# Optimization experiments

Measured on AMD Instinct MI355X. Metric: run time of the kernel, lower is better.

The kernel has to match this reference:

```python
import jax, jax.numpy as jnp
import numpy as np

N = 100000   # nodes
E = 1600000  # edges
D = 128      # in_channels
H = 128      # hidden_dim
L = 3        # num_layers
LH = 128     # lstm_hidden
OUT = 16     # output_dim
G = 128      # graphs in batch
EPS = 1e-5   # BatchNorm eps


def setup_inputs() -> dict:
    key = jax.random.key(0)
    ks = jax.random.split(key, 14)
    x = jax.random.normal(ks[0], (N, D), jnp.float32)
    src = jax.random.randint(ks[1], (E,), 0, N)
    dst = jax.random.randint(ks[2], (E,), 0, N)
    edge_index = jnp.stack([src, dst])
    batch = jnp.sort(jax.random.randint(ks[3], (N,), 0, G))
    Ws = jax.random.normal(ks[4], (L, D, H), jnp.float32) / np.float32(np.sqrt(D))
    bs = jax.random.normal(ks[5], (L, H), jnp.float32) * 0.02
    gammas = 1.0 + 0.1 * jax.random.normal(ks[6], (L, H), jnp.float32)
    betas = 0.1 * jax.random.normal(ks[7], (L, H), jnp.float32)
    rms = 0.1 * jax.random.normal(ks[8], (L, H), jnp.float32)
    rvs = jax.random.uniform(ks[9], (L, H), jnp.float32, 0.5, 1.5)
    W_ih = jax.random.normal(ks[10], (4 * LH, H), jnp.float32) / np.float32(np.sqrt(H))
    W_hh = jax.random.normal(ks[11], (4 * LH, LH), jnp.float32) / np.float32(np.sqrt(LH))
    b_ih = jnp.zeros((4 * LH,), jnp.float32)
    b_hh = jnp.zeros((4 * LH,), jnp.float32)
    W_fc = jax.random.normal(ks[12], (OUT, LH), jnp.float32) / np.float32(np.sqrt(LH))
    b_fc = 0.02 * jax.random.normal(ks[13], (OUT,), jnp.float32)
    return dict(x=x, edge_index=edge_index, batch=batch, Ws=Ws, bs=bs,
                gammas=gammas, betas=betas, rms=rms, rvs=rvs,
                W_ih=W_ih, W_hh=W_hh, b_ih=b_ih, b_hh=b_hh, W_fc=W_fc, b_fc=b_fc)


def reference(x, edge_index, batch, Ws, bs, gammas, betas, rms, rvs,
              W_ih, W_hh, b_ih, b_hh, W_fc, b_fc):
    # GCNConv: add self-loops, symmetric deg^-1/2 normalization
    src, dst = edge_index[0], edge_index[1]
    loop = jnp.arange(N)
    s = jnp.concatenate([src, loop])
    d = jnp.concatenate([dst, loop])
    deg = jax.ops.segment_sum(jnp.ones((E + N,), x.dtype), d, num_segments=N)
    dinv = jax.lax.rsqrt(jnp.maximum(deg, 1.0))  # deg >= 1 due to self-loops
    norm = (dinv[s] * dinv[d])[:, None]          # [E+N, 1]
    h = x
    for l in range(L):
        h = h @ Ws[l]                                                  # [N, H]
        agg = jax.ops.segment_sum(h[s] * norm, d, num_segments=N) + bs[l]
        # BatchNorm (eval: running stats) -> dropout (eval: identity) -> ReLU
        y = (agg - rms[l]) * (gammas[l] * jax.lax.rsqrt(rvs[l] + EPS)) + betas[l]
        h = jax.nn.relu(y)
    # global_mean_pool
    sums = jax.ops.segment_sum(h, batch, num_segments=G)               # [G, H]
    cnt = jax.ops.segment_sum(jnp.ones((N,), h.dtype), batch, num_segments=G)
    pooled = sums / jnp.maximum(cnt, 1.0)[:, None]
    # single-timestep LSTM, h0 = c0 = 0 -> forget gate contributes nothing
    gates = pooled @ W_ih.T + b_ih + b_hh                              # [G, 4*LH]
    i, f, g, o = jnp.split(gates, 4, axis=-1)
    c = jax.nn.sigmoid(i) * jnp.tanh(g)
    hn = jax.nn.sigmoid(o) * jnp.tanh(c)
    return hn @ W_fc.T + b_fc                                          # [G, OUT]
```

## Files before the change

### kernel.cpp

```cpp
#include <hip/hip_runtime.h>
#include <math.h>

constexpr int   NN  = 100000;
constexpr int   EE  = 1600000;
constexpr int   HH  = 128;
constexpr int   GG  = 128;
constexpr float EPSV = 1e-5f;
constexpr int   NSB = 256;
constexpr int   SUBW = (NN + NSB - 1) / NSB;
constexpr int   CAP2 = 8192;
constexpr int   GEMM_BLOCKS = (NN + 127) / 128;

typedef __attribute__((ext_vector_type(8))) short  short8;
typedef __attribute__((ext_vector_type(4))) float  f32x4;
typedef __attribute__((ext_vector_type(2))) float  v2f;

__device__ __forceinline__ unsigned short f2bf(float f) {
    union { float f; unsigned u; } v; v.f = f;
    unsigned r = v.u + 0x7FFF + ((v.u >> 16) & 1);
    return (unsigned short)(r >> 16);
}
__device__ __forceinline__ float bf2f(unsigned short b) {
    union { unsigned u; float f; } v; v.u = ((unsigned)b) << 16;
    return v.f;
}

constexpr size_t A256(size_t x) { return (x + 255) & ~(size_t)255; }
constexpr size_t OFF_TL  = 0;
constexpr size_t OFF_DNV = A256(OFF_TL  + 256 * 4);
constexpr size_t OFF_RP  = A256(OFF_DNV + (size_t)NN * 4);
constexpr size_t OFF_SRC = A256(OFF_RP  + (size_t)(NN + 1) * 4);
constexpr size_t OFF_B2  = A256(OFF_SRC + (size_t)EE * 4);
constexpr size_t OFF_HW  = A256(OFF_B2  + (size_t)NSB * CAP2 * 4);
constexpr size_t OFF_H0  = A256(OFF_HW  + (size_t)NN * HH * 2);
constexpr size_t OFF_PL  = A256(OFF_H0  + (size_t)NN * HH * 2);

template<bool FP32A>
__device__ __forceinline__ void gemm_body(const void* __restrict__ Ap,
                                          const float* __restrict__ W,
                                          unsigned short* __restrict__ C,
                                          int nrows, int rb) {
    __shared__ unsigned short WtH[64 * 136];
    __shared__ unsigned short WtL[64 * 136];
    int t = threadIdx.x;
    int row0 = rb * 128;
    int wv = t >> 6, lane = t & 63, m = lane & 15, q = lane >> 4;
    long rowA = row0 + wv * 32 + m;
    long rowB = rowA + 16;

    short8 a[2][4];
#pragma unroll
    for (int kc = 0; kc < 4; ++kc) {
        int ko = kc * 32 + q * 8;
        if (FP32A) {
            const float* Af = (const float*)Ap;
            float4 f0 = {0,0,0,0}, f1 = {0,0,0,0}, g0 = {0,0,0,0}, g1 = {0,0,0,0};
            if (rowA < nrows) {
                f0 = *(const float4*)(Af + rowA * 128 + ko);
                f1 = *(const float4*)(Af + rowA * 128 + ko + 4);
            }
            if (rowB < nrows) {
                g0 = *(const float4*)(Af + rowB * 128 + ko);
                g1 = *(const float4*)(Af + rowB * 128 + ko + 4);
            }
            union { short8 s; unsigned short u[8]; } ua, ub;
            ua.u[0] = f2bf(f0.x); ua.u[1] = f2bf(f0.y); ua.u[2] = f2bf(f0.z); ua.u[3] = f2bf(f0.w);
            ua.u[4] = f2bf(f1.x); ua.u[5] = f2bf(f1.y); ua.u[6] = f2bf(f1.z); ua.u[7] = f2bf(f1.w);
            ub.u[0] = f2bf(g0.x); ub.u[1] = f2bf(g0.y); ub.u[2] = f2bf(g0.z); ub.u[3] = f2bf(g0.w);
            ub.u[4] = f2bf(g1.x); ub.u[5] = f2bf(g1.y); ub.u[6] = f2bf(g1.z); ub.u[7] = f2bf(g1.w);
            a[0][kc] = ua.s; a[1][kc] = ub.s;
        } else {
            const unsigned short* Ab = (const unsigned short*)Ap;
            short8 z = {};
            a[0][kc] = (rowA < nrows) ? *(const short8*)(Ab + rowA * 128 + ko) : z;
            a[1][kc] = (rowB < nrows) ? *(const short8*)(Ab + rowB * 128 + ko) : z;
        }
    }

    for (int half = 0; half < 2; ++half) {
        int c0 = half * 64;
        __syncthreads();
        for (int idx = t; idx < 64 * 128; idx += 256) {
            int k = idx >> 6, c = idx & 63;
            float w = W[k * 128 + c0 + c];
            unsigned short hb = f2bf(w);
            WtH[c * 136 + k] = hb;
            WtL[c * 136 + k] = f2bf(w - bf2f(hb));
        }
        __syncthreads();
        f32x4 acc[2][4] = {};
#pragma unroll
        for (int kc = 0; kc < 4; ++kc) {
            int ko = kc * 32 + q * 8;
#pragma unroll
            for (int ct = 0; ct < 4; ++ct) {
                short8 bh = *(const short8*)(WtH + (ct * 16 + m) * 136 + ko);
                short8 bl = *(const short8*)(WtL + (ct * 16 + m) * 136 + ko);
                acc[0][ct] = __builtin_amdgcn_mfma_f32_16x16x32_bf16(a[0][kc], bh, acc[0][ct], 0, 0, 0);
                acc[0][ct] = __builtin_amdgcn_mfma_f32_16x16x32_bf16(a[0][kc], bl, acc[0][ct], 0, 0, 0);
                acc[1][ct] = __builtin_amdgcn_mfma_f32_16x16x32_bf16(a[1][kc], bh, acc[1][ct], 0, 0, 0);
                acc[1][ct] = __builtin_amdgcn_mfma_f32_16x16x32_bf16(a[1][kc], bl, acc[1][ct], 0, 0, 0);
            }
        }
        __syncthreads();
        unsigned short* Cs = WtH;
#pragma unroll
        for (int rt = 0; rt < 2; ++rt)
#pragma unroll
            for (int ct = 0; ct < 4; ++ct)
#pragma unroll
                for (int r = 0; r < 4; ++r) {
                    int rl = wv * 32 + rt * 16 + q * 4 + r;
                    Cs[rl * 68 + ct * 16 + m] = f2bf(acc[rt][ct][r]);
                }
        __syncthreads();
        for (int idx = t; idx < 128 * 16; idx += 256) {
            int row = idx >> 4, ch = idx & 15;
            long grow = row0 + row;
            if (grow < nrows)
                *(ushort4*)(C + grow * 128 + c0 + ch * 4) = *(const ushort4*)(Cs + row * 68 + ch * 4);
        }
    }
}

__device__ void binall_body(const int* __restrict__ src, const int* __restrict__ dst,
                            unsigned* __restrict__ bins2, unsigned* __restrict__ tail2,
                            int b) {
    __shared__ unsigned cnt[NSB];
    __shared__ unsigned cur[NSB];
    int t = threadIdx.x;
    cnt[t] = 0;
    __syncthreads();
    const int nvec = EE / 4;
    int csz = (nvec + NSB - 1) / NSB;
    int i0 = b * csz;
    int i1 = i0 + csz; if (i1 > nvec) i1 = nvec;
    const int4* d4 = (const int4*)dst;
    const int4* s4 = (const int4*)src;
    for (int i = i0 + t; i < i1; i += 256) {
        int4 d = d4[i];
        atomicAdd(&cnt[(unsigned)d.x / SUBW], 1u);
        atomicAdd(&cnt[(unsigned)d.y / SUBW], 1u);
        atomicAdd(&cnt[(unsigned)d.z / SUBW], 1u);
        atomicAdd(&cnt[(unsigned)d.w / SUBW], 1u);
    }
    __syncthreads();
    cur[t] = atomicAdd(&tail2[t], cnt[t]);
    __syncthreads();
    for (int i = i0 + t; i < i1; i += 256) {
        int4 d = d4[i];
        int4 s = s4[i];
        int dd[4] = {d.x, d.y, d.z, d.w};
        int ss[4] = {s.x, s.y, s.z, s.w};
#pragma unroll
        for (int c = 0; c < 4; ++c) {
            unsigned gsb = (unsigned)dd[c] / SUBW;
            unsigned p = atomicAdd(&cur[gsb], 1u);
            if (p < (unsigned)CAP2)
                bins2[(size_t)gsb * CAP2 + p] =
                    ((unsigned)(dd[c] - gsb * SUBW) << 17) | (unsigned)ss[c];
        }
    }
}

__global__ __launch_bounds__(256) void k_gemm0_bin(const float* __restrict__ x,
                                                   const float* __restrict__ W,
                                                   unsigned short* __restrict__ C,
                                                   const int* __restrict__ src,
                                                   const int* __restrict__ dst,
                                                   unsigned* __restrict__ bins2,
                                                   unsigned* __restrict__ tail2) {
    if (blockIdx.x < GEMM_BLOCKS)
        gemm_body<true>(x, W, C, NN, blockIdx.x);
    else
        binall_body(src, dst, bins2, tail2, blockIdx.x - GEMM_BLOCKS);
}

__global__ __launch_bounds__(256) void k_gemm(const unsigned short* __restrict__ A,
                                              const float* __restrict__ W,
                                              unsigned short* __restrict__ C) {
    gemm_body<false>(A, W, C, NN, blockIdx.x);
}

__global__ __launch_bounds__(256) void k_build(const unsigned* __restrict__ bins2,
                                               const unsigned* __restrict__ tail2,
                                               int* __restrict__ rp,
                                               float* __restrict__ dinv,
                                               int* __restrict__ ssrc,
                                               float* __restrict__ pooled) {
    __shared__ int hist[SUBW];
    __shared__ int sa[512], sd[512];
    __shared__ unsigned ta[256], tb[256];
    int b = blockIdx.x, t = threadIdx.x;

    if (b < 65) {
        int idx = b * 256 + t;
        if (idx < GG * HH + GG) pooled[idx] = 0.f;
    }

    unsigned v = tail2[t];
    ta[t] = v;
    __syncthreads();
    unsigned *sp = ta, *dp = tb;
    for (int off = 1; off < 256; off <<= 1) {
        dp[t] = sp[t] + ((t >= off) ? sp[t - off] : 0u);
        __syncthreads();
        unsigned* tmp = sp; sp = dp; dp = tmp;
    }
    unsigned base = sp[b] - tail2[b];
    unsigned m = tail2[b];
    if (m > (unsigned)CAP2) m = CAP2;

    int lo = b * SUBW;
    int nn = NN - lo; if (nn > SUBW) nn = SUBW;
    for (int i = t; i < nn; i += 256) hist[i] = 0;
    __syncthreads();

    const unsigned* bb = bins2 + (size_t)b * CAP2;
    unsigned nv = m >> 2;
    for (unsigned i = t; i < nv; i += 256) {
        uint4 u = ((const uint4*)bb)[i];
        atomicAdd(&hist[u.x >> 17], 1);
        atomicAdd(&hist[u.y >> 17], 1);
        atomicAdd(&hist[u.z >> 17], 1);
        atomicAdd(&hist[u.w >> 17], 1);
    }
    for (unsigned i = (m & ~3u) + t; i < m; i += 256)
        atomicAdd(&hist[bb[i] >> 17], 1);
    __syncthreads();

    sa[t]       = (t < nn)       ? hist[t]       : 0;
    sa[t + 256] = (t + 256 < nn) ? hist[t + 256] : 0;
    __syncthreads();
    int* s = sa; int* d = sd;
    for (int off = 1; off < 512; off <<= 1) {
        d[t]       = s[t]       + ((t >= off)       ? s[t - off]       : 0);
        d[t + 256] = s[t + 256] + ((t + 256 >= off) ? s[t + 256 - off] : 0);
        __syncthreads();
        int* tmp = s; s = d; d = tmp;
    }

    for (int i = t; i < nn; i += 256) {
        int cur0 = (int)base + (i ? s[i - 1] : 0);
        rp[lo + i]   = cur0;
        dinv[lo + i] = rsqrtf((float)(hist[i] + 1));
    }
    __syncthreads();
    for (int i = t; i < nn; i += 256)
        hist[i] = (int)base + (i ? s[i - 1] : 0);
    if (b == 255 && t == 0) rp[NN] = EE;
    __syncthreads();

    for (unsigned i = t; i < nv; i += 256) {
        uint4 u = ((const uint4*)bb)[i];
        int p;
        p = atomicAdd(&hist[u.x >> 17], 1); ssrc[p] = (int)(u.x & 0x1FFFFu);
        p = atomicAdd(&hist[u.y >> 17], 1); ssrc[p] = (int)(u.y & 0x1FFFFu);
        p = atomicAdd(&hist[u.z >> 17], 1); ssrc[p] = (int)(u.z & 0x1FFFFu);
        p = atomicAdd(&hist[u.w >> 17], 1); ssrc[p] = (int)(u.w & 0x1FFFFu);
    }
    for (unsigned i = (m & ~3u) + t; i < m; i += 256) {
        unsigned u = bb[i];
        int p = atomicAdd(&hist[u >> 17], 1);
        ssrc[p] = (int)(u & 0x1FFFFu);
    }
}

__global__ __launch_bounds__(256) void k_agg(const unsigned short* __restrict__ hw,
                                             const int* __restrict__ rp,
                                             const int* __restrict__ ssrc,
                                             const float* __restrict__ dinv,
                                             const float* __restrict__ bsl,
                                             const float* __restrict__ gamma,
                                             const float* __restrict__ beta,
                                             const float* __restrict__ rm,
                                             const float* __restrict__ rv,
                                             unsigned short* __restrict__ out) {
    int lane = threadIdx.x & 63;
    int c2   = lane * 2;
    int n = blockIdx.x * 4 + (threadIdx.x >> 6);
    if (n >= NN) return;
    int beg = rp[n], end = rp[n + 1];

    v2f acc0 = {0.f, 0.f}, acc1 = {0.f, 0.f};

    for (int chunk = beg; chunk < end; chunk += 64) {
        int l = chunk + lane;
        bool valid = (l < end);
        int   e  = valid ? ssrc[l] : n;
        float dv = valid ? dinv[e] : 0.f;
        int cnt = end - chunk;
        if (cnt > 64) cnt = 64;
        for (int jb = 0; jb < cnt; jb += 8) {
#pragma unroll
            for (int j = 0; j < 8; ++j) {
                int s    = __builtin_amdgcn_readlane(e, jb + j);
                float ds = __int_as_float(
                               __builtin_amdgcn_readlane(__float_as_int(dv), jb + j));
                unsigned u = *(const unsigned*)(hw + (size_t)s * HH + c2);
                v2f vv;
                vv.x = __int_as_float((int)(u << 16));
                vv.y = __int_as_float((int)(u & 0xffff0000u));
                v2f d2 = {ds, ds};
                if (j & 1) acc1 += d2 * vv;
                else       acc0 += d2 * vv;
            }
        }
    }
    v2f a = acc0 + acc1;

    float di = dinv[n];
    {
        unsigned u = *(const unsigned*)(hw + (size_t)n * HH + c2);
        v2f vv;
        vv.x = __int_as_float((int)(u << 16));
        vv.y = __int_as_float((int)(u & 0xffff0000u));
        v2f d2 = {di, di};
        a += d2 * vv;
    }
    a.x *= di;
    a.y *= di;

    float g0 = gamma[c2],   g1 = gamma[c2 + 1];
    float r0 = rv[c2],      r1 = rv[c2 + 1];
    float s0 = g0 * rsqrtf(r0 + EPSV);
    float s1 = g1 * rsqrtf(r1 + EPSV);
    float b0 = fmaf(bsl[c2]     - rm[c2],     s0, beta[c2]);
    float b1 = fmaf(bsl[c2 + 1] - rm[c2 + 1], s1, beta[c2 + 1]);
    float y0 = fmaxf(fmaf(a.x, s0, b0), 0.f);
    float y1 = fmaxf(fmaf(a.y, s1, b1), 0.f);
    ushort2 o;
    o.x = f2bf(y0);
    o.y = f2bf(y1);
    *(ushort2*)(out + (size_t)n * HH + c2) = o;
}

__global__ __launch_bounds__(128) void k_pool(const unsigned short* __restrict__ h,
                                              const int* __restrict__ batch,
                                              float* __restrict__ pooled,
                                              float* __restrict__ cnt) {
    int t = threadIdx.x;
    const int chunk = (NN + 1023) / 1024;
    int n0 = blockIdx.x * chunk;
    if (n0 >= NN) return;
    int n1 = n0 + chunk;
    if (n1 > NN) n1 = NN;
    int cur = batch[n0];
    float acc = 0.f;
    int k = 0;
    for (int n = n0; n < n1; ++n) {
        int b = batch[n];
        if (b != cur) {
            atomicAdd(&pooled[(size_t)cur * 128 + t], acc);
            if (t == 0) atomicAdd(&cnt[cur], (float)k);
            acc = 0.f; k = 0; cur = b;
        }
        acc += bf2f(h[(size_t)n * 128 + t]);
        ++k;
    }
    atomicAdd(&pooled[(size_t)cur * 128 + t], acc);
    if (t == 0) atomicAdd(&cnt[cur], (float)k);
}

__global__ __launch_bounds__(128) void k_head(const float* __restrict__ pooled,
                                              const float* __restrict__ cnt,
                                              const float* __restrict__ W_ih,
                                              const float* __restrict__ b_ih,
                                              const float* __restrict__ b_hh,
                                              const float* __restrict__ W_fc,
                                              const float* __restrict__ b_fc,
                                              float* __restrict__ out) {
    __shared__ float pm[128];
    __shared__ float gate[512];
    __shared__ float hn[128];
    int g = blockIdx.x, t = threadIdx.x;
    float cdiv = fmaxf(cnt[g], 1.0f);
    pm[t] = pooled[(size_t)g * 128 + t] / cdiv;
    __syncthreads();
    for (int j = t; j < 512; j += 128) {
        float acc = b_ih[j] + b_hh[j];
        const float* w = W_ih + (size_t)j * 128;
#pragma unroll 8
        for (int k = 0; k < 128; ++k) acc = fmaf(pm[k], w[k], acc);
        gate[j] = acc;
    }
    __syncthreads();
    {
        float gi = gate[t], gg = gate[256 + t], go = gate[384 + t];
        float cc = (1.f / (1.f + expf(-gi))) * tanhf(gg);
        hn[t] = (1.f / (1.f + expf(-go))) * tanhf(cc);
    }
    __syncthreads();
    if (t < 16) {
        float acc = b_fc[t];
        const float* w = W_fc + (size_t)t * 128;
#pragma unroll 8
        for (int k = 0; k < 128; ++k) acc = fmaf(hn[k], w[k], acc);
        out[(size_t)g * 16 + t] = acc;
    }
}

extern "C" void kernel_launch(void* const* d_in, const int* in_sizes, int n_in,
                              void* d_out, int out_size, void* d_ws, size_t ws_size,
                              hipStream_t stream) {
    const float* x      = (const float*)d_in[0];
    const int*   ei     = (const int*)d_in[1];
    const int*   src    = ei;
    const int*   dst    = ei + EE;
    const int*   batch  = (const int*)d_in[2];
    const float* Ws     = (const float*)d_in[3];
    const float* bs     = (const float*)d_in[4];
    const float* gammas = (const float*)d_in[5];
    const float* betas  = (const float*)d_in[6];
    const float* rms    = (const float*)d_in[7];
    const float* rvs    = (const float*)d_in[8];
    const float* W_ih   = (const float*)d_in[9];
    const float* b_ih   = (const float*)d_in[11];
    const float* b_hh   = (const float*)d_in[12];
    const float* W_fc   = (const float*)d_in[13];
    const float* b_fc   = (const float*)d_in[14];
    float* out = (float*)d_out;

    char* w = (char*)d_ws;
    unsigned*       tail2  = (unsigned*)(w + OFF_TL);
    float*          dinv   = (float*)(w + OFF_DNV);
    int*            rp     = (int*)(w + OFF_RP);
    int*            ssrc   = (int*)(w + OFF_SRC);
    unsigned*       bins2  = (unsigned*)(w + OFF_B2);
    unsigned short* hwb    = (unsigned short*)(w + OFF_HW);
    unsigned short* h0     = (unsigned short*)(w + OFF_H0);
    float*          pooled = (float*)(w + OFF_PL);
    float*          cntb   = pooled + (size_t)GG * HH;

    hipMemsetAsync(tail2, 0, 256 * 4, stream);

    k_gemm0_bin<<<GEMM_BLOCKS + NSB, 256, 0, stream>>>(x, Ws, hwb, src, dst, bins2, tail2);
    k_build<<<NSB, 256, 0, stream>>>(bins2, tail2, rp, dinv, ssrc, pooled);

    for (int l = 0; l < 3; ++l) {
        if (l > 0)
            k_gemm<<<GEMM_BLOCKS, 256, 0, stream>>>(h0, Ws + (size_t)l * 128 * 128, hwb);
        k_agg<<<(NN + 3) / 4, 256, 0, stream>>>(hwb, rp, ssrc, dinv,
                                                bs + l * 128, gammas + l * 128, betas + l * 128,
                                                rms + l * 128, rvs + l * 128, h0);
    }
    k_pool<<<1024, 128, 0, stream>>>(h0, batch, pooled, cntb);
    k_head<<<GG, 128, 0, stream>>>(pooled, cntb, W_ih, b_ih, b_hh, W_fc, b_fc, out);
}
```

Measured before the change: 443.2 us.

## Pack edge src and dinv into one array; gather 16-byte rows per lane group

Adds a pass that precomputes, for every edge, a packed (source index, dinv[source]) pair, so the aggregation kernel reads one uint2 per edge instead of an index plus a dependent dinv gather. The aggregation kernel is restructured so each wave processes four edges at once, with each 16-lane group loading a full 256-byte bf16 row as 16-byte vectors, followed by a cross-group shuffle reduction. This is meant to cut dependent gather latency and raise memory-level parallelism per instruction. In exchange it adds an extra 12.8 MB workspace array and an extra kernel launch, and the reduction and epilogue work is done redundantly or masked to one group.

```diff
diff --git a/kernel.cpp b/kernel.cpp
--- a/kernel.cpp
+++ b/kernel.cpp
@@ -24,6 +24,12 @@
     union { unsigned u; float f; } v; v.u = ((unsigned)b) << 16;
     return v.f;
 }
+__device__ __forceinline__ v2f unpk(unsigned u) {
+    v2f r;
+    r.x = __int_as_float((int)(u << 16));
+    r.y = __int_as_float((int)(u & 0xffff0000u));
+    return r;
+}
 
 constexpr size_t A256(size_t x) { return (x + 255) & ~(size_t)255; }
 constexpr size_t OFF_TL  = 0;
@@ -31,7 +37,8 @@
 constexpr size_t OFF_RP  = A256(OFF_DNV + (size_t)NN * 4);
 constexpr size_t OFF_SRC = A256(OFF_RP  + (size_t)(NN + 1) * 4);
 constexpr size_t OFF_B2  = A256(OFF_SRC + (size_t)EE * 4);
-constexpr size_t OFF_HW  = A256(OFF_B2  + (size_t)NSB * CAP2 * 4);
+constexpr size_t OFF_ED  = A256(OFF_B2  + (size_t)NSB * CAP2 * 4);
+constexpr size_t OFF_HW  = A256(OFF_ED  + (size_t)EE * 8);
 constexpr size_t OFF_H0  = A256(OFF_HW  + (size_t)NN * HH * 2);
 constexpr size_t OFF_PL  = A256(OFF_H0  + (size_t)NN * HH * 2);
 
@@ -266,9 +273,18 @@
     }
 }
 
+__global__ void k_edata(const int* __restrict__ ssrc, const float* __restrict__ dinv,
+                        uint2* __restrict__ edata) {
+    int i = blockIdx.x * 256 + threadIdx.x;
+    if (i < EE) {
+        int s = ssrc[i];
+        edata[i] = make_uint2((unsigned)s, __float_as_uint(dinv[s]));
+    }
+}
+
 __global__ __launch_bounds__(256) void k_agg(const unsigned short* __restrict__ hw,
                                              const int* __restrict__ rp,
-                                             const int* __restrict__ ssrc,
+                                             const uint2* __restrict__ edata,
                                              const float* __restrict__ dinv,
                                              const float* __restrict__ bsl,
                                              const float* __restrict__ gamma,
@@ -277,62 +293,73 @@
                                              const float* __restrict__ rv,
                                              unsigned short* __restrict__ out) {
     int lane = threadIdx.x & 63;
-    int c2   = lane * 2;
+    int grp  = lane >> 4;
+    int c8   = (lane & 15) * 8;
     int n = blockIdx.x * 4 + (threadIdx.x >> 6);
-    if (n >= NN) return;
     int beg = rp[n], end = rp[n + 1];
 
-    v2f acc0 = {0.f, 0.f}, acc1 = {0.f, 0.f};
+    v2f a0 = {0.f,0.f}, a1 = {0.f,0.f}, a2 = {0.f,0.f}, a3 = {0.f,0.f};
 
     for (int chunk = beg; chunk < end; chunk += 64) {
         int l = chunk + lane;
-        bool valid = (l < end);
-        int   e  = valid ? ssrc[l] : n;
-        float dv = valid ? dinv[e] : 0.f;
+        uint2 ed = (l < end) ? edata[l] : make_uint2((unsigned)n, 0u);
         int cnt = end - chunk;
         if (cnt > 64) cnt = 64;
-        for (int jb = 0; jb < cnt; jb += 8) {
-#pragma unroll
-            for (int j = 0; j < 8; ++j) {
-                int s    = __builtin_amdgcn_readlane(e, jb + j);
-                float ds = __int_as_float(
-                               __builtin_amdgcn_readlane(__float_as_int(dv), jb + j));
-                unsigned u = *(const unsigned*)(hw + (size_t)s * HH + c2);
-                v2f vv;
-                vv.x = __int_as_float((int)(u << 16));
-                vv.y = __int_as_float((int)(u & 0xffff0000u));
-                v2f d2 = {ds, ds};
-                if (j & 1) acc1 += d2 * vv;
-                else       acc0 += d2 * vv;
-            }
-        }
-    }
-    v2f a = acc0 + acc1;
+#pragma unroll 4
+        for (int jb = 0; jb < cnt; jb += 4) {
+            int srcl = jb + grp;
+            int s    = __shfl((int)ed.x, srcl);
+            float dv = __int_as_float(__shfl((int)ed.y, srcl));
+            uint4 u  = *(const uint4*)(hw + (size_t)s * HH + c8);
+            v2f d2 = {dv, dv};
+            a0 += d2 * unpk(u.x);
+            a1 += d2 * unpk(u.y);
+            a2 += d2 * unpk(u.z);
+            a3 += d2 * unpk(u.w);
+        }
+    }
+#define REDUCE(f) f += __shfl_xor(f, 16); f += __shfl_xor(f, 32)
+    REDUCE(a0.x); REDUCE(a0.y); REDUCE(a1.x); REDUCE(a1.y);
+    REDUCE(a2.x); REDUCE(a2.y); REDUCE(a3.x); REDUCE(a3.y);
+#undef REDUCE
 
     float di = dinv[n];
     {
-        unsigned u = *(const unsigned*)(hw + (size_t)n * HH + c2);
-        v2f vv;
-        vv.x = __int_as_float((int)(u << 16));
-        vv.y = __int_as_float((int)(u & 0xffff0000u));
+        uint4 u = *(const uint4*)(hw + (size_t)n * HH + c8);
         v2f d2 = {di, di};
-        a += d2 * vv;
-    }
-    a.x *= di;
-    a.y *= di;
-
-    float g0 = gamma[c2],   g1 = gamma[c2 + 1];
-    float r0 = rv[c2],      r1 = rv[c2 + 1];
-    float s0 = g0 * rsqrtf(r0 + EPSV);
-    float s1 = g1 * rsqrtf(r1 + EPSV);
-    float b0 = fmaf(bsl[c2]     - rm[c2],     s0, beta[c2]);
-    float b1 = fmaf(bsl[c2 + 1] - rm[c2 + 1], s1, beta[c2 + 1]);
-    float y0 = fmaxf(fmaf(a.x, s0, b0), 0.f);
-    float y1 = fmaxf(fmaf(a.y, s1, b1), 0.f);
-    ushort2 o;
-    o.x = f2bf(y0);
-    o.y = f2bf(y1);
-    *(ushort2*)(out + (size_t)n * HH + c2) = o;
+        a0 += d2 * unpk(u.x);
+        a1 += d2 * unpk(u.y);
+        a2 += d2 * unpk(u.z);
+        a3 += d2 * unpk(u.w);
+    }
+    v2f dd = {di, di};
+    a0 *= dd; a1 *= dd; a2 *= dd; a3 *= dd;
+
+    if (grp == 0) {
+        float4 g0 = *(const float4*)(gamma + c8), g1 = *(const float4*)(gamma + c8 + 4);
+        float4 r0 = *(const float4*)(rv + c8),    r1 = *(const float4*)(rv + c8 + 4);
+        float4 m0 = *(const float4*)(rm + c8),    m1 = *(const float4*)(rm + c8 + 4);
+        float4 t0 = *(const float4*)(beta + c8),  t1 = *(const float4*)(beta + c8 + 4);
+        float4 b0 = *(const float4*)(bsl + c8),   b1 = *(const float4*)(bsl + c8 + 4);
+        float sc[8] = { g0.x * rsqrtf(r0.x + EPSV), g0.y * rsqrtf(r0.y + EPSV),
+                        g0.z * rsqrtf(r0.z + EPSV), g0.w * rsqrtf(r0.w + EPSV),
+                        g1.x * rsqrtf(r1.x + EPSV), g1.y * rsqrtf(r1.y + EPSV),
+                        g1.z * rsqrtf(r1.z + EPSV), g1.w * rsqrtf(r1.w + EPSV) };
+        float bb[8] = { fmaf(b0.x - m0.x, sc[0], t0.x), fmaf(b0.y - m0.y, sc[1], t0.y),
+                        fmaf(b0.z - m0.z, sc[2], t0.z), fmaf(b0.w - m0.w, sc[3], t0.w),
+                        fmaf(b1.x - m1.x, sc[4], t1.x), fmaf(b1.y - m1.y, sc[5], t1.y),
+                        fmaf(b1.z - m1.z, sc[6], t1.z), fmaf(b1.w - m1.w, sc[7], t1.w) };
+        float y[8] = { fmaxf(fmaf(a0.x, sc[0], bb[0]), 0.f), fmaxf(fmaf(a0.y, sc[1], bb[1]), 0.f),
+                       fmaxf(fmaf(a1.x, sc[2], bb[2]), 0.f), fmaxf(fmaf(a1.y, sc[3], bb[3]), 0.f),
+                       fmaxf(fmaf(a2.x, sc[4], bb[4]), 0.f), fmaxf(fmaf(a2.y, sc[5], bb[5]), 0.f),
+                       fmaxf(fmaf(a3.x, sc[6], bb[6]), 0.f), fmaxf(fmaf(a3.y, sc[7], bb[7]), 0.f) };
+        uint4 o;
+        o.x = (unsigned)f2bf(y[0]) | ((unsigned)f2bf(y[1]) << 16);
+        o.y = (unsigned)f2bf(y[2]) | ((unsigned)f2bf(y[3]) << 16);
+        o.z = (unsigned)f2bf(y[4]) | ((unsigned)f2bf(y[5]) << 16);
+        o.w = (unsigned)f2bf(y[6]) | ((unsigned)f2bf(y[7]) << 16);
+        *(uint4*)(out + (size_t)n * HH + c8) = o;
+    }
 }
 
 __global__ __launch_bounds__(128) void k_pool(const unsigned short* __restrict__ h,
@@ -427,6 +454,7 @@
     int*            rp     = (int*)(w + OFF_RP);
     int*            ssrc   = (int*)(w + OFF_SRC);
     unsigned*       bins2  = (unsigned*)(w + OFF_B2);
+    uint2*          edata  = (uint2*)(w + OFF_ED);
     unsigned short* hwb    = (unsigned short*)(w + OFF_HW);
     unsigned short* h0     = (unsigned short*)(w + OFF_H0);
     float*          pooled = (float*)(w + OFF_PL);
@@ -436,11 +464,12 @@
 
     k_gemm0_bin<<<GEMM_BLOCKS + NSB, 256, 0, stream>>>(x, Ws, hwb, src, dst, bins2, tail2);
     k_build<<<NSB, 256, 0, stream>>>(bins2, tail2, rp, dinv, ssrc, pooled);
+    k_edata<<<(EE + 255) / 256, 256, 0, stream>>>(ssrc, dinv, edata);
 
     for (int l = 0; l < 3; ++l) {
         if (l > 0)
             k_gemm<<<GEMM_BLOCKS, 256, 0, stream>>>(h0, Ws + (size_t)l * 128 * 128, hwb);
-        k_agg<<<(NN + 3) / 4, 256, 0, stream>>>(hwb, rp, ssrc, dinv,
+        k_agg<<<(NN + 3) / 4, 256, 0, stream>>>(hwb, rp, edata, dinv,
                                                 bs + l * 128, gammas + l * 128, betas + l * 128,
                                                 rms + l * 128, rvs + l * 128, h0);
     }
```

New measurement: 477.8 us. +7.8%, slower.

## Precompute packed edge (src, dinv) pairs and pre-split bf16 weights

Applied to the files above, without the earlier changes.

Adds a kernel that packs each CSR edge's source index and its source dinv into one 8-byte record, so aggregation loads one uint2 instead of doing a dependent dinv gather per edge in each of three layers. The same kernel also pre-transposes the layer 1-2 weights and splits them into hi/lo bf16 in the shared-memory layout, so each GEMM block just copies them in. This removes the per-block fp32-to-bf16 conversion. It costs an extra launch and about 12.8 MB of extra edge-data traffic to write the packed array.

```diff
diff --git a/kernel.cpp b/kernel.cpp
--- a/kernel.cpp
+++ b/kernel.cpp
@@ -10,6 +10,9 @@
 constexpr int   SUBW = (NN + NSB - 1) / NSB;
 constexpr int   CAP2 = 8192;
 constexpr int   GEMM_BLOCKS = (NN + 127) / 128;
+constexpr int   EDATA_BLOCKS = (EE + 255) / 256;
+constexpr int   WHALF = 64 * 136;
+constexpr int   WLAYER = 2 * 2 * WHALF;
 
 typedef __attribute__((ext_vector_type(8))) short  short8;
 typedef __attribute__((ext_vector_type(4))) float  f32x4;
@@ -31,17 +34,21 @@
 constexpr size_t OFF_RP  = A256(OFF_DNV + (size_t)NN * 4);
 constexpr size_t OFF_SRC = A256(OFF_RP  + (size_t)(NN + 1) * 4);
 constexpr size_t OFF_B2  = A256(OFF_SRC + (size_t)EE * 4);
-constexpr size_t OFF_HW  = A256(OFF_B2  + (size_t)NSB * CAP2 * 4);
+constexpr size_t OFF_ED  = A256(OFF_B2  + (size_t)NSB * CAP2 * 4);
+constexpr size_t OFF_WS  = A256(OFF_ED  + (size_t)EE * 8);
+constexpr size_t OFF_HW  = A256(OFF_WS  + (size_t)2 * WLAYER * 2);
 constexpr size_t OFF_H0  = A256(OFF_HW  + (size_t)NN * HH * 2);
 constexpr size_t OFF_PL  = A256(OFF_H0  + (size_t)NN * HH * 2);
 
 template<bool FP32A>
 __device__ __forceinline__ void gemm_body(const void* __restrict__ Ap,
                                           const float* __restrict__ W,
+                                          const unsigned short* __restrict__ Wsp,
                                           unsigned short* __restrict__ C,
                                           int nrows, int rb) {
-    __shared__ unsigned short WtH[64 * 136];
-    __shared__ unsigned short WtL[64 * 136];
+    __shared__ unsigned short smem[2 * WHALF];
+    unsigned short* WtH = smem;
+    unsigned short* WtL = smem + WHALF;
     int t = threadIdx.x;
     int row0 = rb * 128;
     int wv = t >> 6, lane = t & 63, m = lane & 15, q = lane >> 4;
@@ -80,12 +87,18 @@
     for (int half = 0; half < 2; ++half) {
         int c0 = half * 64;
         __syncthreads();
-        for (int idx = t; idx < 64 * 128; idx += 256) {
-            int k = idx >> 6, c = idx & 63;
-            float w = W[k * 128 + c0 + c];
-            unsigned short hb = f2bf(w);
-            WtH[c * 136 + k] = hb;
-            WtL[c * 136 + k] = f2bf(w - bf2f(hb));
+        if (FP32A) {
+            for (int idx = t; idx < 64 * 128; idx += 256) {
+                int k = idx >> 6, c = idx & 63;
+                float w = W[k * 128 + c0 + c];
+                unsigned short hb = f2bf(w);
+                WtH[c * 136 + k] = hb;
+                WtL[c * 136 + k] = f2bf(w - bf2f(hb));
+            }
+        } else {
+            const uint4* srcw = (const uint4*)(Wsp + (size_t)half * 2 * WHALF);
+            uint4* dstw = (uint4*)smem;
+            for (int i = t; i < 2176; i += 256) dstw[i] = srcw[i];
         }
         __syncthreads();
         f32x4 acc[2][4] = {};
@@ -103,7 +116,7 @@
             }
         }
         __syncthreads();
-        unsigned short* Cs = WtH;
+        unsigned short* Cs = smem;
 #pragma unroll
         for (int rt = 0; rt < 2; ++rt)
 #pragma unroll
@@ -171,15 +184,15 @@
                                                    unsigned* __restrict__ bins2,
                                                    unsigned* __restrict__ tail2) {
     if (blockIdx.x < GEMM_BLOCKS)
-        gemm_body<true>(x, W, C, NN, blockIdx.x);
+        gemm_body<true>(x, W, nullptr, C, NN, blockIdx.x);
     else
         binall_body(src, dst, bins2, tail2, blockIdx.x - GEMM_BLOCKS);
 }
 
 __global__ __launch_bounds__(256) void k_gemm(const unsigned short* __restrict__ A,
-                                              const float* __restrict__ W,
+                                              const unsigned short* __restrict__ Wsp,
                                               unsigned short* __restrict__ C) {
-    gemm_body<false>(A, W, C, NN, blockIdx.x);
+    gemm_body<false>(A, nullptr, Wsp, C, NN, blockIdx.x);
 }
 
 __global__ __launch_bounds__(256) void k_build(const unsigned* __restrict__ bins2,
@@ -266,9 +279,38 @@
     }
 }
 
+__global__ void k_edata(const int* __restrict__ ssrc, const float* __restrict__ dinv,
+                        uint2* __restrict__ edata, const float* __restrict__ Ws,
+                        unsigned short* __restrict__ wsp) {
+    int b = blockIdx.x;
+    if (b < EDATA_BLOCKS) {
+        int i = b * 256 + threadIdx.x;
+        if (i < EE) {
+            int s = ssrc[i];
+            edata[i] = make_uint2((unsigned)s, __float_as_uint(dinv[s]));
+        }
+    } else {
+        int t = threadIdx.x;
+        if (t < 128) {
+            int e = (b - EDATA_BLOCKS) * 128 + t;
+            int l = e >> 14;
+            int r = e & 16383;
+            int k = r >> 7;
+            int c = r & 127;
+            int half = c >> 6, cl = c & 63;
+            float w = Ws[(size_t)(l + 1) * 16384 + k * 128 + c];
+            unsigned short hb = f2bf(w);
+            unsigned short lb = f2bf(w - bf2f(hb));
+            size_t base = (size_t)l * WLAYER + (size_t)half * 2 * WHALF;
+            wsp[base + cl * 136 + k]         = hb;
+            wsp[base + WHALF + cl * 136 + k] = lb;
+        }
+    }
+}
+
 __global__ __launch_bounds__(256) void k_agg(const unsigned short* __restrict__ hw,
                                              const int* __restrict__ rp,
-                                             const int* __restrict__ ssrc,
+                                             const uint2* __restrict__ edata,
                                              const float* __restrict__ dinv,
                                              const float* __restrict__ bsl,
                                              const float* __restrict__ gamma,
@@ -286,9 +328,9 @@
 
     for (int chunk = beg; chunk < end; chunk += 64) {
         int l = chunk + lane;
-        bool valid = (l < end);
-        int   e  = valid ? ssrc[l] : n;
-        float dv = valid ? dinv[e] : 0.f;
+        uint2 ed = (l < end) ? edata[l] : make_uint2((unsigned)n, 0u);
+        int   e  = (int)ed.x;
+        float dv = __uint_as_float(ed.y);
         int cnt = end - chunk;
         if (cnt > 64) cnt = 64;
         for (int jb = 0; jb < cnt; jb += 8) {
@@ -427,6 +469,8 @@
     int*            rp     = (int*)(w + OFF_RP);
     int*            ssrc   = (int*)(w + OFF_SRC);
     unsigned*       bins2  = (unsigned*)(w + OFF_B2);
+    uint2*          edata  = (uint2*)(w + OFF_ED);
+    unsigned short* wsp    = (unsigned short*)(w + OFF_WS);
     unsigned short* hwb    = (unsigned short*)(w + OFF_HW);
     unsigned short* h0     = (unsigned short*)(w + OFF_H0);
     float*          pooled = (float*)(w + OFF_PL);
@@ -436,11 +480,12 @@
 
     k_gemm0_bin<<<GEMM_BLOCKS + NSB, 256, 0, stream>>>(x, Ws, hwb, src, dst, bins2, tail2);
     k_build<<<NSB, 256, 0, stream>>>(bins2, tail2, rp, dinv, ssrc, pooled);
+    k_edata<<<EDATA_BLOCKS + 256, 256, 0, stream>>>(ssrc, dinv, edata, Ws, wsp);
 
     for (int l = 0; l < 3; ++l) {
         if (l > 0)
-            k_gemm<<<GEMM_BLOCKS, 256, 0, stream>>>(h0, Ws + (size_t)l * 128 * 128, hwb);
-        k_agg<<<(NN + 3) / 4, 256, 0, stream>>>(hwb, rp, ssrc, dinv,
+            k_gemm<<<GEMM_BLOCKS, 256, 0, stream>>>(h0, wsp + (size_t)(l - 1) * WLAYER, hwb);
+        k_agg<<<(NN + 3) / 4, 256, 0, stream>>>(hwb, rp, edata, dinv,
                                                 bs + l * 128, gammas + l * 128, betas + l * 128,
                                                 rms + l * 128, rvs + l * 128, h0);
     }
```

Measured after the change: 435.9 us. About the same (-1.6%).
